# Optimization experiments

Measured on AMD Instinct MI355X. Metric: run time of the kernel, lower is better.

The kernel has to match this reference:

```python
import jax, jax.numpy as jnp
import numpy as np

B, N, D, O = 128, 256, 512, 512
EPS = 1e-5


def setup_inputs() -> dict:
    key = jax.random.key(0)
    ks = jax.random.split(key, 12)
    Observation = jax.random.normal(ks[0], (B, N, D), dtype=jnp.float32)
    mask = jax.random.bernoulli(ks[1], 0.7, (B, N))
    s = 0.02
    W1 = jax.random.normal(ks[2], (D, O), dtype=jnp.float32) * s
    W2 = jax.random.normal(ks[3], (O, O), dtype=jnp.float32) * s
    W3 = jax.random.normal(ks[4], (O, O), dtype=jnp.float32) * s
    g1 = 1.0 + 0.1 * jax.random.normal(ks[5], (D,), dtype=jnp.float32)
    b1 = 0.02 * jax.random.normal(ks[6], (D,), dtype=jnp.float32)
    g2 = 1.0 + 0.1 * jax.random.normal(ks[7], (O,), dtype=jnp.float32)
    b2 = 0.02 * jax.random.normal(ks[8], (O,), dtype=jnp.float32)
    g3 = 1.0 + 0.1 * jax.random.normal(ks[9], (O,), dtype=jnp.float32)
    b3 = 0.02 * jax.random.normal(ks[10], (O,), dtype=jnp.float32)
    return {"Observation": Observation, "mask": mask,
            "g1": g1, "b1": b1, "W1": W1,
            "g2": g2, "b2": b2, "W2": W2,
            "g3": g3, "b3": b3, "W3": W3}


def layer_norm(x, g, b):
    m = jnp.mean(x, axis=-1, keepdims=True)
    v = jnp.mean(jnp.square(x - m), axis=-1, keepdims=True)
    return (x - m) * jax.lax.rsqrt(v + EPS) * g + b


def reference(Observation, mask, g1, b1, W1, g2, b2, W2, g3, b3, W3):
    Bv, Nv, Dv = Observation.shape
    # _grant_at_least_one_valid: force element 0 valid if a row is all-invalid
    all_invalid = ~jnp.any(mask, axis=1)  # [B]
    mask = mask | (all_invalid[:, None] & (jnp.arange(Nv) == 0)[None, :])
    x = Observation.reshape(-1, Dv)  # [B*N, D]
    # Block 1: LN -> Linear (no bias) -> Tanh (dropout is eval identity)
    h1 = jnp.tanh(layer_norm(x, g1, b1) @ W1)
    # Block 2
    h2 = jnp.tanh(layer_norm(h1, g2, b2) @ W2)
    # Block 3 with residual input (h2 + h1), no activation
    o3 = layer_norm(h2 + h1, g3, b3) @ W3  # [B*N, O]
    fill = jnp.finfo(o3.dtype).min
    o3 = jnp.where(mask.reshape(-1, 1), o3, fill)
    out = jax.nn.softmax(o3.reshape(Bv, Nv, -1), axis=1)
    return jnp.nan_to_num(out, nan=0.0)
```

## Files before the change

### kernel.cpp

```cpp
#include <hip/hip_runtime.h>


#define NN 256

typedef _Float16 f16;
typedef __attribute__((ext_vector_type(4))) _Float16 f16x4;
typedef __attribute__((ext_vector_type(8))) _Float16 f16x8;
typedef __attribute__((ext_vector_type(4))) float f32x4;

#define XS    520
#define EPS32 516

__device__ __forceinline__ float fast_tanh(float x) {
  float e = __expf(2.f * x);
  return 1.f - 2.f * __builtin_amdgcn_rcpf(e + 1.f);
}

__global__ void prep_w_kernel(const float* __restrict__ W1, const float* __restrict__ W2,
                              const float* __restrict__ W3, f16* __restrict__ WTc) {
  int idx = blockIdx.x * 256 + threadIdx.x;
  int g    = idx >> 18;
  int rem  = idx & 0x3FFFF;
  int c    = rem >> 14;
  int o    = (rem >> 5) & 511;
  int dlow = rem & 31;
  const float* W = (g == 0) ? W1 : (g == 1) ? W2 : W3;
  WTc[idx] = (f16)W[(c * 32 + dlow) * 512 + o];
}

__device__ __forceinline__ void gemm_step(f32x4 acc[4][4], const f16* __restrict__ sXb,
                                          const f16x8 bf[4], int c) {
  f16x8 af[4];
  #pragma unroll
  for (int i = 0; i < 4; ++i)
    af[i] = *(const f16x8*)&sXb[i * 16 * XS + c * 32];
  #pragma unroll
  for (int mi = 0; mi < 4; ++mi)
    #pragma unroll
    for (int ni = 0; ni < 4; ++ni)
      acc[mi][ni] = __builtin_amdgcn_mfma_f32_16x16x32_f16(af[mi], bf[ni], acc[mi][ni], 0, 0, 0);
}

__global__ __launch_bounds__(512, 2) void mega_kernel(
    const float* __restrict__ Obs,
    const float* __restrict__ g1, const float* __restrict__ b1,
    const f16* __restrict__ WTc,
    const float* __restrict__ g2, const float* __restrict__ b2,
    const float* __restrict__ g3, const float* __restrict__ b3,
    float* __restrict__ outF) {
  __shared__ __align__(16) char smem[71168];
  f16* sX = (f16*)smem;
  float2* sPart = (float2*)(smem + 66560);
  float2* sStat = (float2*)(smem + 70656);

  int t = threadIdx.x, lane = t & 63, wv = t >> 6;
  int row16 = lane & 15, quad = lane >> 4;
  int rBase = blockIdx.x * 64;

  const f16* sXb = sX + row16 * XS + quad * 8;
  const f16* bw = WTc + wv * 2048 + row16 * 32 + quad * 8;

  f32x4 acc[4][4];
  f16x8 bfA[4], bfB[4];
  f16x4 h1s[4][4];

  #pragma unroll
  for (int i = 0; i < 4; ++i) bfA[i] = *(const f16x8*)(bw + i * 512);

  {
    float4 w0 = *(const float4*)(g1 + lane * 4);
    float4 u0 = *(const float4*)(b1 + lane * 4);
    float4 w1 = *(const float4*)(g1 + 256 + lane * 4);
    float4 u1 = *(const float4*)(b1 + 256 + lane * 4);
    #pragma unroll
    for (int p = 0; p < 8; ++p) {
      int row = wv * 8 + p;
      const float* x = Obs + (((size_t)(rBase + row)) << 9);
      float4 v0 = *(const float4*)(x + lane * 4);
      float4 v1 = *(const float4*)(x + 256 + lane * 4);
      float s = v0.x + v0.y + v0.z + v0.w + v1.x + v1.y + v1.z + v1.w;
      float q = v0.x*v0.x + v0.y*v0.y + v0.z*v0.z + v0.w*v0.w
              + v1.x*v1.x + v1.y*v1.y + v1.z*v1.z + v1.w*v1.w;
      #pragma unroll
      for (int off = 1; off < 64; off <<= 1) {
        s += __shfl_xor(s, off, 64);
        q += __shfl_xor(q, off, 64);
      }
      float mean = s * (1.f / 512.f);
      float var  = q * (1.f / 512.f) - mean * mean;
      float inv  = 1.f / sqrtf(var + 1e-5f);
      f16x4 o0, o1;
      o0[0] = (f16)((v0.x - mean) * inv * w0.x + u0.x);
      o0[1] = (f16)((v0.y - mean) * inv * w0.y + u0.y);
      o0[2] = (f16)((v0.z - mean) * inv * w0.z + u0.z);
      o0[3] = (f16)((v0.w - mean) * inv * w0.w + u0.w);
      o1[0] = (f16)((v1.x - mean) * inv * w1.x + u1.x);
      o1[1] = (f16)((v1.y - mean) * inv * w1.y + u1.y);
      o1[2] = (f16)((v1.z - mean) * inv * w1.z + u1.z);
      o1[3] = (f16)((v1.w - mean) * inv * w1.w + u1.w);
      *(f16x4*)&sX[row * XS + lane * 4] = o0;
      *(f16x4*)&sX[row * XS + 256 + lane * 4] = o1;
    }
  }
  __syncthreads();

  for (int g = 0; g < 3; ++g) {
    #pragma unroll
    for (int mi = 0; mi < 4; ++mi)
      #pragma unroll
      for (int ni = 0; ni < 4; ++ni)
        acc[mi][ni] = (f32x4){0.f, 0.f, 0.f, 0.f};

    #pragma unroll
    for (int c = 0; c < 16; c += 2) {
      #pragma unroll
      for (int i = 0; i < 4; ++i)
        bfB[i] = *(const f16x8*)(bw + (c + 1) * 16384 + i * 512);
      gemm_step(acc, sXb, bfA, c);
      if (c + 2 < 16) {
        #pragma unroll
        for (int i = 0; i < 4; ++i)
          bfA[i] = *(const f16x8*)(bw + (c + 2) * 16384 + i * 512);
      }
      gemm_step(acc, sXb, bfB, c + 1);
    }

    if (g == 2) {
      __syncthreads();
      float* sE = (float*)smem;
      #pragma unroll
      for (int half = 0; half < 2; ++half) {
        #pragma unroll
        for (int mi = 0; mi < 2; ++mi) {
          int rt = half * 2 + mi;
          #pragma unroll
          for (int ni = 0; ni < 4; ++ni) {
            int col = wv * 64 + ni * 16 + row16;
            #pragma unroll
            for (int rg = 0; rg < 4; ++rg)
              sE[(mi * 16 + quad * 4 + rg) * EPS32 + col] = acc[rt][ni][rg];
          }
        }
        __syncthreads();
        #pragma unroll
        for (int i = 0; i < 8; ++i) {
          int gi = t + i * 512;
          int row = gi >> 7, cg = (gi & 127) * 4;
          f32x4 v = *(const f32x4*)&sE[row * EPS32 + cg];
          *(f32x4*)&outF[(((size_t)(rBase + half * 32 + row)) << 9) + cg] = v;
        }
        __syncthreads();
      }
    } else {
      #pragma unroll
      for (int mi = 0; mi < 4; ++mi)
        #pragma unroll
        for (int ni = 0; ni < 4; ++ni)
          #pragma unroll
          for (int rg = 0; rg < 4; ++rg)
            acc[mi][ni][rg] = fast_tanh(acc[mi][ni][rg]);

      if (g == 0) {
        #pragma unroll
        for (int mi = 0; mi < 4; ++mi)
          #pragma unroll
          for (int ni = 0; ni < 4; ++ni) {
            f16x4 h;
            #pragma unroll
            for (int rg = 0; rg < 4; ++rg) h[rg] = (f16)acc[mi][ni][rg];
            h1s[mi][ni] = h;
          }
      } else {
        #pragma unroll
        for (int mi = 0; mi < 4; ++mi)
          #pragma unroll
          for (int ni = 0; ni < 4; ++ni)
            #pragma unroll
            for (int rg = 0; rg < 4; ++rg)
              acc[mi][ni][rg] += (float)h1s[mi][ni][rg];
      }

      const float* gp = (g == 0) ? g2 : g3;
      const float* bp = (g == 0) ? b2 : b3;
      float gva[4], bva[4];
      #pragma unroll
      for (int ni = 0; ni < 4; ++ni) {
        int col = wv * 64 + ni * 16 + row16;
        gva[ni] = gp[col]; bva[ni] = bp[col];
      }

      #pragma unroll
      for (int mi = 0; mi < 4; ++mi)
        #pragma unroll
        for (int rg = 0; rg < 4; ++rg) {
          float s = 0.f, q = 0.f;
          #pragma unroll
          for (int ni = 0; ni < 4; ++ni) {
            float v = acc[mi][ni][rg];
            s += v; q += v * v;
          }
          #pragma unroll
          for (int off = 1; off < 16; off <<= 1) {
            s += __shfl_xor(s, off, 16);
            q += __shfl_xor(q, off, 16);
          }
          if (row16 == 0)
            sPart[wv * 64 + mi * 16 + quad * 4 + rg] = make_float2(s, q);
        }
      __syncthreads();
      if (t < 64) {
        float s = 0.f, q = 0.f;
        #pragma unroll
        for (int w = 0; w < 8; ++w) {
          float2 p = sPart[w * 64 + t];
          s += p.x; q += p.y;
        }
        float mean = s * (1.f / 512.f);
        float var  = q * (1.f / 512.f) - mean * mean;
        sStat[t] = make_float2(mean, 1.f / sqrtf(var + 1e-5f));
      }

      bw += 262144;
      #pragma unroll
      for (int i = 0; i < 4; ++i) bfA[i] = *(const f16x8*)(bw + i * 512);

      __syncthreads();

      #pragma unroll
      for (int mi = 0; mi < 4; ++mi)
        #pragma unroll
        for (int rg = 0; rg < 4; ++rg) {
          int row = mi * 16 + quad * 4 + rg;
          float2 st = sStat[row];
          #pragma unroll
          for (int ni = 0; ni < 4; ++ni) {
            int col = wv * 64 + ni * 16 + row16;
            sX[row * XS + col] = (f16)((acc[mi][ni][rg] - st.x) * st.y * gva[ni] + bva[ni]);
          }
        }
      __syncthreads();
    }
  }
}

__global__ __launch_bounds__(256, 2) void softmax_kernel(const float* __restrict__ o3,
                                                         const int* __restrict__ mask,
                                                         float* __restrict__ out) {
  __shared__ float4 smx[16][16];
  __shared__ float4 sms[16][16];
  __shared__ int    smask[NN];

  int b  = blockIdx.x >> 3;
  int oc = blockIdx.x & 7;
  int t  = threadIdx.x;
  int c4 = t & 15;
  int nh = t >> 4;

  const float4* src = (const float4*)(o3 + (((size_t)(b * NN)) << 9)) + oc * 16 + c4;
  float4 v[16];
  #pragma unroll
  for (int j = 0; j < 16; ++j)
    v[j] = src[(size_t)(nh + 16 * j) * 128];

  int mt = mask[b * NN + t];
  int any = __syncthreads_or(mt);
  smask[t] = (t == 0 && !any) ? 1 : mt;
  __syncthreads();

  const float NEG = -3.4e38f;
  #pragma unroll
  for (int j = 0; j < 16; ++j)
    if (!smask[nh + 16 * j]) v[j] = (float4){NEG, NEG, NEG, NEG};

  float4 m4 = v[0];
  #pragma unroll
  for (int j = 1; j < 16; ++j) {
    m4.x = fmaxf(m4.x, v[j].x); m4.y = fmaxf(m4.y, v[j].y);
    m4.z = fmaxf(m4.z, v[j].z); m4.w = fmaxf(m4.w, v[j].w);
  }
  smx[nh][c4] = m4;
  __syncthreads();
  float4 mm = smx[0][c4];
  #pragma unroll
  for (int k = 1; k < 16; ++k) {
    float4 o = smx[k][c4];
    mm.x = fmaxf(mm.x, o.x); mm.y = fmaxf(mm.y, o.y);
    mm.z = fmaxf(mm.z, o.z); mm.w = fmaxf(mm.w, o.w);
  }

  float4 s4 = {0.f, 0.f, 0.f, 0.f};
  #pragma unroll
  for (int j = 0; j < 16; ++j) {
    s4.x += __expf(v[j].x - mm.x); s4.y += __expf(v[j].y - mm.y);
    s4.z += __expf(v[j].z - mm.z); s4.w += __expf(v[j].w - mm.w);
  }
  sms[nh][c4] = s4;
  __syncthreads();
  float4 tot = sms[0][c4];
  #pragma unroll
  for (int k = 1; k < 16; ++k) {
    float4 o = sms[k][c4];
    tot.x += o.x; tot.y += o.y; tot.z += o.z; tot.w += o.w;
  }
  float4 inv = {1.f / tot.x, 1.f / tot.y, 1.f / tot.z, 1.f / tot.w};

  float4* dst = (float4*)(out + (((size_t)(b * NN)) << 9)) + oc * 16 + c4;
  #pragma unroll
  for (int j = 0; j < 16; ++j) {
    float4 r;
    r.x = __expf(v[j].x - mm.x) * inv.x;
    r.y = __expf(v[j].y - mm.y) * inv.y;
    r.z = __expf(v[j].z - mm.z) * inv.z;
    r.w = __expf(v[j].w - mm.w) * inv.w;
    dst[(size_t)(nh + 16 * j) * 128] = r;
  }
}

extern "C" void kernel_launch(void* const* d_in, const int* in_sizes, int n_in,
                              void* d_out, int out_size, void* d_ws, size_t ws_size,
                              hipStream_t stream) {
  const float* Obs = (const float*)d_in[0];
  const int*   msk = (const int*)d_in[1];
  const float* g1  = (const float*)d_in[2];
  const float* b1  = (const float*)d_in[3];
  const float* W1  = (const float*)d_in[4];
  const float* g2  = (const float*)d_in[5];
  const float* b2  = (const float*)d_in[6];
  const float* W2  = (const float*)d_in[7];
  const float* g3  = (const float*)d_in[8];
  const float* b3  = (const float*)d_in[9];
  const float* W3  = (const float*)d_in[10];
  float* out = (float*)d_out;

  char* ws = (char*)d_ws;
  const size_t MB = 1u << 20;
  float* Lg = (float*)ws;
  f16*   WTc = (f16*)(ws + 64 * MB);

  prep_w_kernel<<<3072, 256, 0, stream>>>(W1, W2, W3, WTc);
  mega_kernel<<<512, 512, 0, stream>>>(Obs, g1, b1, WTc, g2, b2, g3, b3, Lg);
  softmax_kernel<<<1024, 256, 0, stream>>>(Lg, msk, out);
}
```

Baseline: 279.0 us.

## Split mega kernel across 16 waves in 2x8 grid with rotated K order

Doubles the block to 1024 threads, arranging waves as 2 row groups by 8 column groups so each wave computes a 32x64 tile instead of 64x64. This halves per-wave accumulators and A-fragment loads, and adds a per-block rotation of the K-chunk start so different blocks read different weight chunks at the same time. The intent is more waves in flight to hide memory and LDS latency, and less contention on the same weight lines in L2. The cost is that every wave now reloads the full B fragments for only half the rows, which doubles global weight traffic per block, and the launch bound of 4 blocks of 1024 threads may not fit given the shared memory use.

After: 377.7 us. 1.35x slower.

```diff
diff --git a/kernel.cpp b/kernel.cpp
--- a/kernel.cpp
+++ b/kernel.cpp
@@ -28,20 +28,20 @@
   WTc[idx] = (f16)W[(c * 32 + dlow) * 512 + o];
 }
 
-__device__ __forceinline__ void gemm_step(f32x4 acc[4][4], const f16* __restrict__ sXb,
+__device__ __forceinline__ void gemm_step(f32x4 acc[2][4], const f16* __restrict__ sXb,
                                           const f16x8 bf[4], int c) {
-  f16x8 af[4];
-  #pragma unroll
-  for (int i = 0; i < 4; ++i)
+  f16x8 af[2];
+  #pragma unroll
+  for (int i = 0; i < 2; ++i)
     af[i] = *(const f16x8*)&sXb[i * 16 * XS + c * 32];
   #pragma unroll
-  for (int mi = 0; mi < 4; ++mi)
+  for (int mi = 0; mi < 2; ++mi)
     #pragma unroll
     for (int ni = 0; ni < 4; ++ni)
       acc[mi][ni] = __builtin_amdgcn_mfma_f32_16x16x32_f16(af[mi], bf[ni], acc[mi][ni], 0, 0, 0);
 }
 
-__global__ __launch_bounds__(512, 2) void mega_kernel(
+__global__ __launch_bounds__(1024, 4) void mega_kernel(
     const float* __restrict__ Obs,
     const float* __restrict__ g1, const float* __restrict__ b1,
     const f16* __restrict__ WTc,
@@ -54,18 +54,21 @@
   float2* sStat = (float2*)(smem + 70656);
 
   int t = threadIdx.x, lane = t & 63, wv = t >> 6;
+  int wn = wv & 7, wm = wv >> 3;
   int row16 = lane & 15, quad = lane >> 4;
   int rBase = blockIdx.x * 64;
-
-  const f16* sXb = sX + row16 * XS + quad * 8;
-  const f16* bw = WTc + wv * 2048 + row16 * 32 + quad * 8;
-
-  f32x4 acc[4][4];
+  int rot = blockIdx.x & 15;
+
+  const f16* sXb = sX + (wm * 32 + row16) * XS + quad * 8;
+  const f16* bw  = WTc + (wn * 64 + row16) * 32 + quad * 8;
+
+  f32x4 acc[2][4];
   f16x8 bfA[4], bfB[4];
-  f16x4 h1s[4][4];
-
-  #pragma unroll
-  for (int i = 0; i < 4; ++i) bfA[i] = *(const f16x8*)(bw + i * 512);
+  f16x4 h1s[2][4];
+
+  #pragma unroll
+  for (int ni = 0; ni < 4; ++ni)
+    bfA[ni] = *(const f16x8*)(bw + rot * 16384 + ni * 512);
 
   {
     float4 w0 = *(const float4*)(g1 + lane * 4);
@@ -73,8 +76,8 @@
     float4 w1 = *(const float4*)(g1 + 256 + lane * 4);
     float4 u1 = *(const float4*)(b1 + 256 + lane * 4);
     #pragma unroll
-    for (int p = 0; p < 8; ++p) {
-      int row = wv * 8 + p;
+    for (int p = 0; p < 4; ++p) {
+      int row = wv * 4 + p;
       const float* x = Obs + (((size_t)(rBase + row)) << 9);
       float4 v0 = *(const float4*)(x + lane * 4);
       float4 v1 = *(const float4*)(x + 256 + lane * 4);
@@ -105,24 +108,29 @@
   __syncthreads();
 
   for (int g = 0; g < 3; ++g) {
+    const f16* bg = bw + (size_t)g * 262144;
+
     #pragma unroll
-    for (int mi = 0; mi < 4; ++mi)
+    for (int mi = 0; mi < 2; ++mi)
       #pragma unroll
       for (int ni = 0; ni < 4; ++ni)
         acc[mi][ni] = (f32x4){0.f, 0.f, 0.f, 0.f};
 
     #pragma unroll
-    for (int c = 0; c < 16; c += 2) {
-      #pragma unroll
-      for (int i = 0; i < 4; ++i)
-        bfB[i] = *(const f16x8*)(bw + (c + 1) * 16384 + i * 512);
-      gemm_step(acc, sXb, bfA, c);
-      if (c + 2 < 16) {
-        #pragma unroll
-        for (int i = 0; i < 4; ++i)
-          bfA[i] = *(const f16x8*)(bw + (c + 2) * 16384 + i * 512);
-      }
-      gemm_step(acc, sXb, bfB, c + 1);
+    for (int i = 0; i < 16; i += 2) {
+      int ca = (rot + i) & 15;
+      int cb = (rot + i + 1) & 15;
+      #pragma unroll
+      for (int ni = 0; ni < 4; ++ni)
+        bfB[ni] = *(const f16x8*)(bg + cb * 16384 + ni * 512);
+      gemm_step(acc, sXb, bfA, ca);
+      if (i + 2 < 16) {
+        int cc = (rot + i + 2) & 15;
+        #pragma unroll
+        for (int ni = 0; ni < 4; ++ni)
+          bfA[ni] = *(const f16x8*)(bg + cc * 16384 + ni * 512);
+      }
+      gemm_step(acc, sXb, bfB, cb);
     }
 
     if (g == 2) {
@@ -130,21 +138,21 @@
       float* sE = (float*)smem;
       #pragma unroll
       for (int half = 0; half < 2; ++half) {
-        #pragma unroll
-        for (int mi = 0; mi < 2; ++mi) {
-          int rt = half * 2 + mi;
-          #pragma unroll
-          for (int ni = 0; ni < 4; ++ni) {
-            int col = wv * 64 + ni * 16 + row16;
+        if (wm == half) {
+          #pragma unroll
+          for (int mi = 0; mi < 2; ++mi)
             #pragma unroll
-            for (int rg = 0; rg < 4; ++rg)
-              sE[(mi * 16 + quad * 4 + rg) * EPS32 + col] = acc[rt][ni][rg];
-          }
+            for (int ni = 0; ni < 4; ++ni) {
+              int col = wn * 64 + ni * 16 + row16;
+              #pragma unroll
+              for (int rg = 0; rg < 4; ++rg)
+                sE[(mi * 16 + quad * 4 + rg) * EPS32 + col] = acc[mi][ni][rg];
+            }
         }
         __syncthreads();
         #pragma unroll
-        for (int i = 0; i < 8; ++i) {
-          int gi = t + i * 512;
+        for (int i = 0; i < 4; ++i) {
+          int gi = t + i * 1024;
           int row = gi >> 7, cg = (gi & 127) * 4;
           f32x4 v = *(const f32x4*)&sE[row * EPS32 + cg];
           *(f32x4*)&outF[(((size_t)(rBase + half * 32 + row)) << 9) + cg] = v;
@@ -153,7 +161,7 @@
       }
     } else {
       #pragma unroll
-      for (int mi = 0; mi < 4; ++mi)
+      for (int mi = 0; mi < 2; ++mi)
         #pragma unroll
         for (int ni = 0; ni < 4; ++ni)
           #pragma unroll
@@ -162,7 +170,7 @@
 
       if (g == 0) {
         #pragma unroll
-        for (int mi = 0; mi < 4; ++mi)
+        for (int mi = 0; mi < 2; ++mi)
           #pragma unroll
           for (int ni = 0; ni < 4; ++ni) {
             f16x4 h;
@@ -172,7 +180,7 @@
           }
       } else {
         #pragma unroll
-        for (int mi = 0; mi < 4; ++mi)
+        for (int mi = 0; mi < 2; ++mi)
           #pragma unroll
           for (int ni = 0; ni < 4; ++ni)
             #pragma unroll
@@ -185,12 +193,12 @@
       float gva[4], bva[4];
       #pragma unroll
       for (int ni = 0; ni < 4; ++ni) {
-        int col = wv * 64 + ni * 16 + row16;
+        int col = wn * 64 + ni * 16 + row16;
         gva[ni] = gp[col]; bva[ni] = bp[col];
       }
 
       #pragma unroll
-      for (int mi = 0; mi < 4; ++mi)
+      for (int mi = 0; mi < 2; ++mi)
         #pragma unroll
         for (int rg = 0; rg < 4; ++rg) {
           float s = 0.f, q = 0.f;
@@ -205,14 +213,15 @@
             q += __shfl_xor(q, off, 16);
           }
           if (row16 == 0)
-            sPart[wv * 64 + mi * 16 + quad * 4 + rg] = make_float2(s, q);
+            sPart[wv * 32 + mi * 16 + quad * 4 + rg] = make_float2(s, q);
         }
       __syncthreads();
       if (t < 64) {
+        int wmr = t >> 5, lr = t & 31;
         float s = 0.f, q = 0.f;
         #pragma unroll
         for (int w = 0; w < 8; ++w) {
-          float2 p = sPart[w * 64 + t];
+          float2 p = sPart[(wmr * 8 + w) * 32 + lr];
           s += p.x; q += p.y;
         }
         float mean = s * (1.f / 512.f);
@@ -220,21 +229,21 @@
         sStat[t] = make_float2(mean, 1.f / sqrtf(var + 1e-5f));
       }
 
-      bw += 262144;
-      #pragma unroll
-      for (int i = 0; i < 4; ++i) bfA[i] = *(const f16x8*)(bw + i * 512);
+      #pragma unroll
+      for (int ni = 0; ni < 4; ++ni)
+        bfA[ni] = *(const f16x8*)(bw + (size_t)(g + 1) * 262144 + rot * 16384 + ni * 512);
 
       __syncthreads();
 
       #pragma unroll
-      for (int mi = 0; mi < 4; ++mi)
+      for (int mi = 0; mi < 2; ++mi)
         #pragma unroll
         for (int rg = 0; rg < 4; ++rg) {
-          int row = mi * 16 + quad * 4 + rg;
+          int row = wm * 32 + mi * 16 + quad * 4 + rg;
           float2 st = sStat[row];
           #pragma unroll
           for (int ni = 0; ni < 4; ++ni) {
-            int col = wv * 64 + ni * 16 + row16;
+            int col = wn * 64 + ni * 16 + row16;
             sX[row * XS + col] = (f16)((acc[mi][ni][rg] - st.x) * st.y * gva[ni] + bva[ni]);
           }
         }
@@ -338,6 +347,6 @@
   f16*   WTc = (f16*)(ws + 64 * MB);
 
   prep_w_kernel<<<3072, 256, 0, stream>>>(W1, W2, W3, WTc);
-  mega_kernel<<<512, 512, 0, stream>>>(Obs, g1, b1, WTc, g2, b2, g3, b3, Lg);
+  mega_kernel<<<512, 1024, 0, stream>>>(Obs, g1, b1, WTc, g2, b2, g3, b3, Lg);
   softmax_kernel<<<1024, 256, 0, stream>>>(Lg, msk, out);
 }
```
